# Optimization experiments

Hardware: AMD Instinct MI355X
Metric: run time of the kernel (lower is better)

Reference implementation:

```python
import jax, jax.numpy as jnp
import numpy as np

H = 1024      # hidden_size
NH = 16       # num_attention_heads
HD = H // NH  # head_size
DF = 4096     # ff intermediate
EPS = 1e-5


def layer_norm(x, g, b):
    mu = jnp.mean(x, axis=-1, keepdims=True)
    var = jnp.var(x, axis=-1, keepdims=True)
    return (x - mu) * jax.lax.rsqrt(var + EPS) * g + b


def setup_inputs() -> dict:
    key = jax.random.key(0)
    ks = jax.random.split(key, 4)
    s = 0.02
    return {
        "x": jax.random.normal(ks[0], (2, 2048, H), dtype=jnp.float32),
        "w_qkv": jax.random.normal(ks[1], (H, 3 * H), dtype=jnp.float32) * s,
        "ln1_g": jnp.ones((H,), jnp.float32),
        "ln1_b": jnp.zeros((H,), jnp.float32),
        "w1": jax.random.normal(ks[2], (H, DF), dtype=jnp.float32) * s,
        "b1": jnp.zeros((DF,), jnp.float32),
        "w2": jax.random.normal(ks[3], (DF, H), dtype=jnp.float32) * s,
        "b2": jnp.zeros((H,), jnp.float32),
        "ln2_g": jnp.ones((H,), jnp.float32),
        "ln2_b": jnp.zeros((H,), jnp.float32),
    }


def reference(x, w_qkv, ln1_g, ln1_b, w1, b1, w2, b2, ln2_g, ln2_b):
    b, s, h = x.shape
    # --- MHSelfAttention (naive) ---
    qkv = x @ w_qkv                                   # [b, s, 3h]
    qkv = qkv.reshape(b, s, 3, NH, HD)
    q, k, v = (jnp.moveaxis(qkv, 2, 0)                # [3, b, s, nh, hd]
               .transpose(0, 1, 3, 2, 4))             # [3, b, nh, s, hd]
    # NOTE: faithful quirk — scaled by sqrt(hidden_size), not head_size
    scores = jnp.einsum('bnqd,bnkd->bnqk', q, k) / jnp.sqrt(jnp.float32(h))
    probs = jax.nn.softmax(scores, axis=-1)
    ctx = jnp.einsum('bnqk,bnkd->bnqd', probs, v)     # [b, nh, s, hd]
    attn_out = ctx.transpose(0, 2, 1, 3).reshape(b, s, h)
    # post-norm residual (dropout = identity in eval)
    x = x + layer_norm(attn_out, ln1_g, ln1_b)
    # --- FFN ---
    ff = jax.nn.relu(x @ w1 + b1) @ w2 + b2
    x = x + layer_norm(ff, ln2_g, ln2_b)
    return x
```

## Files before the change

### kernel.cpp

```cpp
#include <hip/hip_runtime.h>


typedef unsigned short u16;
typedef unsigned int u32;
typedef __bf16 bf16x8 __attribute__((ext_vector_type(8)));
typedef float f32x4 __attribute__((ext_vector_type(4)));
typedef float f32x16 __attribute__((ext_vector_type(16)));
typedef u32 u32x4 __attribute__((ext_vector_type(4)));
typedef u16 u16x4 __attribute__((ext_vector_type(4)));

__device__ __forceinline__ u16 f2b(float f) {
  u32 u = __builtin_bit_cast(u32, f);
  u += 0x7fffu + ((u >> 16) & 1u);
  return (u16)(u >> 16);
}
__device__ __forceinline__ float b2f(u16 u) {
  return __builtin_bit_cast(float, (u32)u << 16);
}

__device__ __forceinline__ u32 cvtpk(float lo, float hi) {
  u32 r;
  asm("v_cvt_pk_bf16_f32 %0, %1, %2" : "=v"(r) : "v"(lo), "v"(hi));
  return r;
}

__device__ __forceinline__ void gld_lds16(const u16* g, u16* l) {
  __builtin_amdgcn_global_load_lds(
      (const __attribute__((address_space(1))) u32*)g,
      (__attribute__((address_space(3))) u32*)l, 16, 0, 0);
}

__global__ __launch_bounds__(256) void convert_bf16_kernel(
    const float* __restrict__ in, u16* __restrict__ out) {
  const int idx = blockIdx.x * 256 + threadIdx.x;
  float4 v = ((const float4*)in)[idx];
  u16x4 o = { f2b(v.x), f2b(v.y), f2b(v.z), f2b(v.w) };
  ((u16x4*)out)[idx] = o;
}

__global__ __launch_bounds__(256) void transpose_bf16_kernel(
    const float* __restrict__ in, u16* __restrict__ out, int R, int C) {
  __shared__ float tile[32][33];
  const int cb = blockIdx.x * 32, rb = blockIdx.y * 32;
  const int c = threadIdx.x & 31;
  const int r0 = threadIdx.x >> 5;
#pragma unroll
  for (int rr = 0; rr < 32; rr += 8)
    tile[r0 + rr][c] = in[(size_t)(rb + r0 + rr) * C + cb + c];
  __syncthreads();
#pragma unroll
  for (int rr = 0; rr < 32; rr += 8)
    out[(size_t)(cb + r0 + rr) * R + rb + c] = f2b(tile[c][r0 + rr]);
}

__global__ __launch_bounds__(256) void transpose_v_kernel(
    const u16* __restrict__ qkv, u16* __restrict__ vt) {
  __shared__ u16 t[64][70];
  const int bh = blockIdx.x, st = blockIdx.y;
  const int b = bh >> 4, nh = bh & 15;
  const int s0 = st * 64;
  const int r = threadIdx.x >> 3, c = (threadIdx.x & 7) << 3;
  const u16* src = qkv + (size_t)(b * 2048 + s0) * 3072 + 2048 + nh * 64;
#pragma unroll
  for (int rr = 0; rr < 64; rr += 32)
    *(u32x4*)&t[r + rr][c] = *(const u32x4*)(src + (size_t)(r + rr) * 3072 + c);
  __syncthreads();
  u16* dst = vt + ((size_t)bh * 64) * 2048 + s0;
#pragma unroll
  for (int rr = 0; rr < 64; rr += 32) {
    const int d = r + rr;
    u16 tmp[8];
#pragma unroll
    for (int j = 0; j < 8; ++j) tmp[j] = t[c + j][d];
    *(u32x4*)(dst + (size_t)d * 2048 + c) = *(u32x4*)tmp;
  }
}

__global__ __launch_bounds__(256) void gemm_bt_kernel(
    const u16* __restrict__ A, const u16* __restrict__ Bt,
    const float* __restrict__ bias, float* __restrict__ Cf, u16* __restrict__ Cb,
    int M, int N, int K, int relu,
    u16* __restrict__ Cb1, u16* __restrict__ Cb2, u16* __restrict__ Cb3) {
  const int bid = blockIdx.x;
  const int xcd = bid & 7;
  const int g = bid >> 3;
  const int m0 = (xcd * 4 + (g & 3)) * 128;
  const int n0 = (g >> 2) * 128;
  const int z = blockIdx.y;
  const int kn = K / (int)gridDim.y;
  if (z == 1) Cb = Cb1; else if (z == 2) Cb = Cb2; else if (z == 3) Cb = Cb3;
  const int tid = threadIdx.x;
  const int w = tid >> 6, lane = tid & 63, quad = lane >> 4, l16 = lane & 15;
  const int wm = (w & 1) * 64, wn = (w >> 1) * 64;

  __shared__ u16 As[2][128][32];
  __shared__ u16 Bs[2][128][32];

  f32x4 acc[4][4];
#pragma unroll
  for (int i = 0; i < 4; ++i)
#pragma unroll
    for (int j = 0; j < 4; ++j) acc[i][j] = {0.f, 0.f, 0.f, 0.f};

  const int srow = w * 16 + (lane >> 2);
  const int scol = (lane & 3) << 3;
  const u16* Ag = A + (size_t)(m0 + srow) * K + scol + (size_t)z * kn;
  const u16* Bg = Bt + (size_t)(n0 + srow) * K + scol + (size_t)z * kn;
  const size_t rstep = (size_t)64 * K;

  for (int k0 = 0; k0 < kn; k0 += 64) {
    __syncthreads();
    gld_lds16(Ag + k0,              &As[0][w * 16][0]);
    gld_lds16(Ag + k0 + 32,         &As[1][w * 16][0]);
    gld_lds16(Ag + rstep + k0,      &As[0][64 + w * 16][0]);
    gld_lds16(Ag + rstep + k0 + 32, &As[1][64 + w * 16][0]);
    gld_lds16(Bg + k0,              &Bs[0][w * 16][0]);
    gld_lds16(Bg + k0 + 32,         &Bs[1][w * 16][0]);
    gld_lds16(Bg + rstep + k0,      &Bs[0][64 + w * 16][0]);
    gld_lds16(Bg + rstep + k0 + 32, &Bs[1][64 + w * 16][0]);
    __syncthreads();

#pragma unroll
    for (int s = 0; s < 2; ++s) {
      bf16x8 af[4], bfr[4];
#pragma unroll
      for (int i = 0; i < 4; ++i)
        af[i] = *(const bf16x8*)&As[s][wm + i * 16 + l16][quad * 8];
#pragma unroll
      for (int j = 0; j < 4; ++j)
        bfr[j] = *(const bf16x8*)&Bs[s][wn + j * 16 + l16][quad * 8];
#pragma unroll
      for (int i = 0; i < 4; ++i)
#pragma unroll
        for (int j = 0; j < 4; ++j)
          acc[i][j] = __builtin_amdgcn_mfma_f32_16x16x32_bf16(af[i], bfr[j], acc[i][j], 0, 0, 0);
    }
  }

#pragma unroll
  for (int i = 0; i < 4; ++i) {
    const int row = m0 + wm + i * 16 + quad * 4;
#pragma unroll
    for (int j = 0; j < 4; ++j) {
      const int col = n0 + wn + j * 16 + l16;
      const float bv = bias ? bias[col] : 0.f;
#pragma unroll
      for (int r = 0; r < 4; ++r) {
        float v = acc[i][j][r] + bv;
        if (relu) v = fmaxf(v, 0.f);
        const size_t idx = (size_t)(row + r) * N + col;
        if (Cf) Cf[idx] = v;
        if (Cb) Cb[idx] = f2b(v);
      }
    }
  }
}

__global__ __launch_bounds__(256, 4) void attn_kernel(
    const u16* __restrict__ qkv, const u16* __restrict__ vt,
    float* __restrict__ Op0, float* __restrict__ Op1,
    float* __restrict__ lpart) {
  const int bh = blockIdx.x;
  const int qt = blockIdx.y;
  const int kz = blockIdx.z;
  const int b = bh >> 4, nh = bh & 15;
  const int tid = threadIdx.x;
  const int w = tid >> 6, lane = tid & 63;
  const int l32 = lane & 31, hi = lane >> 5;
  const float c2 = 0.04508422f;

  __shared__ u16 KS[64][64];
  __shared__ u16 VS[64][64];

  const size_t rs = 3072;
  const u16* qbase = qkv + (size_t)b * 2048 * rs + nh * 64;
  const u16* kbase = qbase + 1024;
  const u16* vbase = vt + (size_t)bh * 64 * 2048;
  const int q0 = qt * 128;
  const int k0beg = kz * 1024;

  bf16x8 aq[4];
  {
    const u16* qrow = qbase + (size_t)(q0 + w * 32 + l32) * rs + hi * 8;
#pragma unroll
    for (int ds = 0; ds < 4; ++ds) {
      u32x4 v = *(const u32x4*)(qrow + ds * 16);
      u16 ti[8], to[8];
      *(u32x4*)ti = v;
#pragma unroll
      for (int j = 0; j < 8; ++j) to[j] = f2b(b2f(ti[j]) * c2);
      u32x4 pk = *(u32x4*)to;
      aq[ds] = __builtin_bit_cast(bf16x8, pk);
    }
  }

  f32x16 Oacc[2];
#pragma unroll
  for (int dn = 0; dn < 2; ++dn)
#pragma unroll
    for (int i = 0; i < 16; ++i) Oacc[dn][i] = 0.f;
  float ls[4] = {0.f, 0.f, 0.f, 0.f};

  const int srow = lane >> 3;
  const int scol = ((lane & 7) ^ srow) << 3;

#pragma unroll 1
  for (int t = 0; t < 16; ++t) {
    const int k0 = k0beg + t * 64;
    __syncthreads();
    gld_lds16(kbase + (size_t)(k0 + w * 16 + srow) * rs + scol,       &KS[w * 16][0]);
    gld_lds16(kbase + (size_t)(k0 + w * 16 + 8 + srow) * rs + scol,   &KS[w * 16 + 8][0]);
    gld_lds16(vbase + (size_t)(w * 16 + srow) * 2048 + k0 + scol,     &VS[w * 16][0]);
    gld_lds16(vbase + (size_t)(w * 16 + 8 + srow) * 2048 + k0 + scol, &VS[w * 16 + 8][0]);
    __syncthreads();

    f32x16 S[2];
#pragma unroll
    for (int jt = 0; jt < 2; ++jt)
#pragma unroll
      for (int i = 0; i < 16; ++i) S[jt][i] = 0.f;
#pragma unroll
    for (int jt = 0; jt < 2; ++jt) {
      const int krow = jt * 32 + l32;
#pragma unroll
      for (int ds = 0; ds < 4; ++ds) {
        bf16x8 kv = *(const bf16x8*)&KS[krow][((2 * ds + hi) ^ (krow & 7)) << 3];
        S[jt] = __builtin_amdgcn_mfma_f32_32x32x16_bf16(kv, aq[ds], S[jt], 0, 0, 0);
      }
    }

    bf16x8 pa[4];
#pragma unroll
    for (int jt = 0; jt < 2; ++jt) {
      float p[16];
#pragma unroll
      for (int r = 0; r < 16; ++r) {
        p[r] = exp2f(S[jt][r]);
        ls[r & 3] += p[r];
      }
#pragma unroll
      for (int bq = 0; bq < 2; ++bq) {
        u32 x0 = cvtpk(p[8 * bq + 0], p[8 * bq + 1]);
        u32 y0 = cvtpk(p[8 * bq + 4], p[8 * bq + 5]);
        u32 x1 = cvtpk(p[8 * bq + 2], p[8 * bq + 3]);
        u32 y1 = cvtpk(p[8 * bq + 6], p[8 * bq + 7]);
        asm("v_permlane32_swap_b32 %0, %1" : "+v"(x0), "+v"(y0));
        asm("v_permlane32_swap_b32 %0, %1" : "+v"(x1), "+v"(y1));
        u32x4 dw = {x0, x1, y0, y1};
        pa[2 * jt + bq] = __builtin_bit_cast(bf16x8, dw);
      }
    }

#pragma unroll
    for (int dn = 0; dn < 2; ++dn) {
      const int vrow = dn * 32 + l32;
#pragma unroll
      for (int ks = 0; ks < 4; ++ks) {
        bf16x8 vv = *(const bf16x8*)&VS[vrow][((2 * ks + hi) ^ (vrow & 7)) << 3];
        Oacc[dn] = __builtin_amdgcn_mfma_f32_32x32x16_bf16(pa[ks], vv, Oacc[dn], 0, 0, 0);
      }
    }
  }

  float lsum = (ls[0] + ls[1]) + (ls[2] + ls[3]);
  const float ltot = lsum + __shfl_xor(lsum, 32);

  float* opart = kz ? Op1 : Op0;
  float* obase = opart + (size_t)b * 2048 * 1024 + (size_t)nh * 64;
  float* lbase = lpart + (size_t)kz * 4096 * 16 + (size_t)b * 2048 * 16 + nh;
#pragma unroll
  for (int r = 0; r < 16; ++r) {
    const int qrow = q0 + w * 32 + (r & 3) + 8 * (r >> 2) + 4 * hi;
#pragma unroll
    for (int dn = 0; dn < 2; ++dn)
      obase[(size_t)qrow * 1024 + dn * 32 + l32] = Oacc[dn][r];
  }
  if (lane < 32) lbase[(size_t)(q0 + w * 32 + l32) * 16] = ltot;
}

__global__ __launch_bounds__(256) void ln_attn_kernel(
    const float* __restrict__ O0, const float* __restrict__ O1,
    const float* __restrict__ l0, const float* __restrict__ l1,
    const float* __restrict__ xres, const float* __restrict__ g,
    const float* __restrict__ bb, float* __restrict__ outf,
    u16* __restrict__ outb) {
  const int row = blockIdx.x;
  const int tid = threadIdx.x;
  const int w = tid >> 6, lane = tid & 63;
  const int head = tid >> 4;
  float4 a0 = ((const float4*)(O0 + (size_t)row * 1024))[tid];
  float4 a1 = ((const float4*)(O1 + (size_t)row * 1024))[tid];
  const float inv = 1.f / (l0[row * 16 + head] + l1[row * 16 + head]);
  float4 v;
  v.x = (a0.x + a1.x) * inv;
  v.y = (a0.y + a1.y) * inv;
  v.z = (a0.z + a1.z) * inv;
  v.w = (a0.w + a1.w) * inv;
  float s = v.x + v.y + v.z + v.w;
  float s2 = v.x * v.x + v.y * v.y + v.z * v.z + v.w * v.w;
#pragma unroll
  for (int off = 32; off > 0; off >>= 1) {
    s += __shfl_xor(s, off);
    s2 += __shfl_xor(s2, off);
  }
  __shared__ float red[8];
  if (lane == 0) { red[w] = s; red[4 + w] = s2; }
  __syncthreads();
  s = red[0] + red[1] + red[2] + red[3];
  s2 = red[4] + red[5] + red[6] + red[7];
  const float mu = s * (1.f / 1024.f);
  const float var = s2 * (1.f / 1024.f) - mu * mu;
  const float rstd = rsqrtf(var + 1e-5f);
  float4 xr = ((const float4*)(xres + (size_t)row * 1024))[tid];
  float4 gv = ((const float4*)g)[tid];
  float4 bv = ((const float4*)bb)[tid];
  float4 o;
  o.x = xr.x + (v.x - mu) * rstd * gv.x + bv.x;
  o.y = xr.y + (v.y - mu) * rstd * gv.y + bv.y;
  o.z = xr.z + (v.z - mu) * rstd * gv.z + bv.z;
  o.w = xr.w + (v.w - mu) * rstd * gv.w + bv.w;
  ((float4*)(outf + (size_t)row * 1024))[tid] = o;
  u16x4 ob = { f2b(o.x), f2b(o.y), f2b(o.z), f2b(o.w) };
  *(u16x4*)(outb + (size_t)row * 1024 + (size_t)tid * 4) = ob;
}

__global__ __launch_bounds__(256) void ln_ffn_kernel(
    const u16* __restrict__ p0, const u16* __restrict__ p1,
    const u16* __restrict__ p2, const u16* __restrict__ p3,
    const float* __restrict__ bias, const float* __restrict__ xres,
    const float* __restrict__ g, const float* __restrict__ bb,
    float* __restrict__ outf) {
  const int row = blockIdx.x;
  const int tid = threadIdx.x;
  const int w = tid >> 6, lane = tid & 63;
  u16x4 a0 = ((const u16x4*)(p0 + (size_t)row * 1024))[tid];
  u16x4 a1 = ((const u16x4*)(p1 + (size_t)row * 1024))[tid];
  u16x4 a2 = ((const u16x4*)(p2 + (size_t)row * 1024))[tid];
  u16x4 a3 = ((const u16x4*)(p3 + (size_t)row * 1024))[tid];
  float4 bv4 = ((const float4*)bias)[tid];
  float4 v;
  v.x = (b2f(a0[0]) + b2f(a1[0])) + (b2f(a2[0]) + b2f(a3[0])) + bv4.x;
  v.y = (b2f(a0[1]) + b2f(a1[1])) + (b2f(a2[1]) + b2f(a3[1])) + bv4.y;
  v.z = (b2f(a0[2]) + b2f(a1[2])) + (b2f(a2[2]) + b2f(a3[2])) + bv4.z;
  v.w = (b2f(a0[3]) + b2f(a1[3])) + (b2f(a2[3]) + b2f(a3[3])) + bv4.w;
  float s = v.x + v.y + v.z + v.w;
  float s2 = v.x * v.x + v.y * v.y + v.z * v.z + v.w * v.w;
#pragma unroll
  for (int off = 32; off > 0; off >>= 1) {
    s += __shfl_xor(s, off);
    s2 += __shfl_xor(s2, off);
  }
  __shared__ float red[8];
  if (lane == 0) { red[w] = s; red[4 + w] = s2; }
  __syncthreads();
  s = red[0] + red[1] + red[2] + red[3];
  s2 = red[4] + red[5] + red[6] + red[7];
  const float mu = s * (1.f / 1024.f);
  const float var = s2 * (1.f / 1024.f) - mu * mu;
  const float rstd = rsqrtf(var + 1e-5f);
  float4 xr = ((const float4*)(xres + (size_t)row * 1024))[tid];
  float4 gv = ((const float4*)g)[tid];
  float4 bv = ((const float4*)bb)[tid];
  float4 o;
  o.x = xr.x + (v.x - mu) * rstd * gv.x + bv.x;
  o.y = xr.y + (v.y - mu) * rstd * gv.y + bv.y;
  o.z = xr.z + (v.z - mu) * rstd * gv.z + bv.z;
  o.w = xr.w + (v.w - mu) * rstd * gv.w + bv.w;
  ((float4*)(outf + (size_t)row * 1024))[tid] = o;
}

extern "C" void kernel_launch(void* const* d_in, const int* in_sizes, int n_in,
                              void* d_out, int out_size, void* d_ws, size_t ws_size,
                              hipStream_t stream) {
  const float* x     = (const float*)d_in[0];
  const float* w_qkv = (const float*)d_in[1];
  const float* ln1_g = (const float*)d_in[2];
  const float* ln1_b = (const float*)d_in[3];
  const float* w1    = (const float*)d_in[4];
  const float* b1    = (const float*)d_in[5];
  const float* w2    = (const float*)d_in[6];
  const float* b2    = (const float*)d_in[7];
  const float* ln2_g = (const float*)d_in[8];
  const float* ln2_b = (const float*)d_in[9];
  float* out = (float*)d_out;
  char* ws = (char*)d_ws;

  u16*   xb    = (u16*)(ws + 0);
  u16*   wqkvT = (u16*)(ws + 8388608);
  u16*   qkvb  = (u16*)(ws + 31457280);
  u16*   vT    = (u16*)(ws + 56623104);
  float* Op0   = (float*)(ws + 0);
  float* Op1   = (float*)(ws + 73400320);
  float* lp    = (float*)(ws + 90177536);
  float* x1    = (float*)(ws + 31457280);
  u16*   x1b   = (u16*)(ws + 48234496);
  u16*   w1T   = (u16*)(ws + 14680064);
  u16*   w2T   = (u16*)(ws + 23068672);
  u16*   h1    = (u16*)(ws + 56623104);
  u16*   fp0   = (u16*)(ws + 0);
  u16*   fp1   = (u16*)(ws + 8388608);
  u16*   fp2   = (u16*)(ws + 48234496);
  u16*   fp3   = (u16*)(ws + 90177536);

  convert_bf16_kernel<<<4096, 256, 0, stream>>>(x, xb);
  transpose_bf16_kernel<<<dim3(96, 32), 256, 0, stream>>>(w_qkv, wqkvT, 1024, 3072);

  gemm_bt_kernel<<<dim3(32 * 24, 1), 256, 0, stream>>>(
      xb, wqkvT, nullptr, nullptr, qkvb, 4096, 3072, 1024, 0,
      nullptr, nullptr, nullptr);
  transpose_v_kernel<<<dim3(32, 32), 256, 0, stream>>>(qkvb, vT);
  attn_kernel<<<dim3(32, 16, 2), 256, 0, stream>>>(qkvb, vT, Op0, Op1, lp);

  ln_attn_kernel<<<4096, 256, 0, stream>>>(
      Op0, Op1, lp, lp + 4096 * 16, x, ln1_g, ln1_b, x1, x1b);

  transpose_bf16_kernel<<<dim3(128, 32), 256, 0, stream>>>(w1, w1T, 1024, 4096);
  transpose_bf16_kernel<<<dim3(32, 128), 256, 0, stream>>>(w2, w2T, 4096, 1024);

  gemm_bt_kernel<<<dim3(32 * 32, 1), 256, 0, stream>>>(
      x1b, w1T, b1, nullptr, h1, 4096, 4096, 1024, 1,
      nullptr, nullptr, nullptr);
  gemm_bt_kernel<<<dim3(32 * 8, 4), 256, 0, stream>>>(
      h1, w2T, nullptr, nullptr, fp0, 4096, 1024, 4096, 0,
      fp1, fp2, fp3);

  ln_ffn_kernel<<<4096, 256, 0, stream>>>(
      fp0, fp1, fp2, fp3, b2, x1, ln2_g, ln2_b, out);
}
```

Before: 344.8 us.

## Double-buffer K/V LDS tiles in attention kernel to overlap loads with MFMA

The attention kernel now keeps two K and two V tiles in shared memory. It issues the direct global-to-LDS loads for the next key block before computing on the current one, and moves the Q-load prologue to overlap with the first stage. Each iteration now has one wait-and-barrier instead of two __syncthreads, which is meant to hide global load latency behind the QK and PV MFMAs. LDS use doubles to 32 KB per block, which could reduce occupancy relative to the declared 4 blocks per CU.

```diff
diff --git a/kernel.cpp b/kernel.cpp
--- a/kernel.cpp
+++ b/kernel.cpp
@@ -169,8 +169,8 @@
   const int l32 = lane & 31, hi = lane >> 5;
   const float c2 = 0.04508422f;
 
-  __shared__ u16 KS[64][64];
-  __shared__ u16 VS[64][64];
+  __shared__ u16 KS[2][64][64];
+  __shared__ u16 VS[2][64][64];
 
   const size_t rs = 3072;
   const u16* qbase = qkv + (size_t)b * 2048 * rs + nh * 64;
@@ -179,6 +179,18 @@
   const int q0 = qt * 128;
   const int k0beg = kz * 1024;
 
+  const int srow = lane >> 3;
+  const int scol = ((lane & 7) ^ srow) << 3;
+
+  auto stage = [&](int buf, int k0) {
+    gld_lds16(kbase + (size_t)(k0 + w * 16 + srow) * rs + scol,       &KS[buf][w * 16][0]);
+    gld_lds16(kbase + (size_t)(k0 + w * 16 + 8 + srow) * rs + scol,   &KS[buf][w * 16 + 8][0]);
+    gld_lds16(vbase + (size_t)(w * 16 + srow) * 2048 + k0 + scol,     &VS[buf][w * 16][0]);
+    gld_lds16(vbase + (size_t)(w * 16 + 8 + srow) * 2048 + k0 + scol, &VS[buf][w * 16 + 8][0]);
+  };
+
+  stage(0, k0beg);
+
   bf16x8 aq[4];
   {
     const u16* qrow = qbase + (size_t)(q0 + w * 32 + l32) * rs + hi * 8;
@@ -201,18 +213,14 @@
     for (int i = 0; i < 16; ++i) Oacc[dn][i] = 0.f;
   float ls[4] = {0.f, 0.f, 0.f, 0.f};
 
-  const int srow = lane >> 3;
-  const int scol = ((lane & 7) ^ srow) << 3;
-
+  asm volatile("s_waitcnt vmcnt(0)" ::: "memory");
+  __builtin_amdgcn_s_barrier();
+  __builtin_amdgcn_sched_barrier(0);
+
+  int cur = 0;
 #pragma unroll 1
   for (int t = 0; t < 16; ++t) {
-    const int k0 = k0beg + t * 64;
-    __syncthreads();
-    gld_lds16(kbase + (size_t)(k0 + w * 16 + srow) * rs + scol,       &KS[w * 16][0]);
-    gld_lds16(kbase + (size_t)(k0 + w * 16 + 8 + srow) * rs + scol,   &KS[w * 16 + 8][0]);
-    gld_lds16(vbase + (size_t)(w * 16 + srow) * 2048 + k0 + scol,     &VS[w * 16][0]);
-    gld_lds16(vbase + (size_t)(w * 16 + 8 + srow) * 2048 + k0 + scol, &VS[w * 16 + 8][0]);
-    __syncthreads();
+    if (t < 15) stage(cur ^ 1, k0beg + (t + 1) * 64);
 
     f32x16 S[2];
 #pragma unroll
@@ -224,7 +232,7 @@
       const int krow = jt * 32 + l32;
 #pragma unroll
       for (int ds = 0; ds < 4; ++ds) {
-        bf16x8 kv = *(const bf16x8*)&KS[krow][((2 * ds + hi) ^ (krow & 7)) << 3];
+        bf16x8 kv = *(const bf16x8*)&KS[cur][krow][((2 * ds + hi) ^ (krow & 7)) << 3];
         S[jt] = __builtin_amdgcn_mfma_f32_32x32x16_bf16(kv, aq[ds], S[jt], 0, 0, 0);
       }
     }
@@ -256,10 +264,16 @@
       const int vrow = dn * 32 + l32;
 #pragma unroll
       for (int ks = 0; ks < 4; ++ks) {
-        bf16x8 vv = *(const bf16x8*)&VS[vrow][((2 * ks + hi) ^ (vrow & 7)) << 3];
+        bf16x8 vv = *(const bf16x8*)&VS[cur][vrow][((2 * ks + hi) ^ (vrow & 7)) << 3];
         Oacc[dn] = __builtin_amdgcn_mfma_f32_32x32x16_bf16(pa[ks], vv, Oacc[dn], 0, 0, 0);
       }
     }
+
+    __builtin_amdgcn_sched_barrier(0);
+    asm volatile("s_waitcnt vmcnt(0)" ::: "memory");
+    __builtin_amdgcn_s_barrier();
+    __builtin_amdgcn_sched_barrier(0);
+    cur ^= 1;
   }
 
   float lsum = (ls[0] + ls[1]) + (ls[2] + ls[3]);
```

After: 343.7 us. About the same (-0.3%).

## Split attention key range across wave pairs within block, reduce partials in LDS

Applied to the files above, without the earlier changes.

Each attention block now covers 64 query rows instead of 128. Its four waves form two pairs, and each pair walks half of the block's key range with its own K/V LDS buffers. At the end the second pair's O and row-sum partials go through shared memory to the first pair, which adds them and writes out. The grid doubles so the GPU gets more blocks and shorter serial key loops per block, at the cost of a final LDS reduction, twice the LDS footprint, and more total Q loading per K/V tile.

```diff
diff --git a/kernel.cpp b/kernel.cpp
--- a/kernel.cpp
+++ b/kernel.cpp
@@ -166,22 +166,26 @@
   const int b = bh >> 4, nh = bh & 15;
   const int tid = threadIdx.x;
   const int w = tid >> 6, lane = tid & 63;
+  const int qw = w & 1, kp = w >> 1;
   const int l32 = lane & 31, hi = lane >> 5;
   const float c2 = 0.04508422f;
 
-  __shared__ u16 KS[64][64];
-  __shared__ u16 VS[64][64];
+  __shared__ u16 KS[2][64][64];
+  __shared__ u16 VS[2][64][64];
 
   const size_t rs = 3072;
   const u16* qbase = qkv + (size_t)b * 2048 * rs + nh * 64;
   const u16* kbase = qbase + 1024;
   const u16* vbase = vt + (size_t)bh * 64 * 2048;
-  const int q0 = qt * 128;
-  const int k0beg = kz * 1024;
+  const int q0 = qt * 64;
+  const int k0beg = kz * 1024 + kp * 512;
+
+  const int srow = lane >> 3;
+  const int scol = ((lane & 7) ^ srow) << 3;
 
   bf16x8 aq[4];
   {
-    const u16* qrow = qbase + (size_t)(q0 + w * 32 + l32) * rs + hi * 8;
+    const u16* qrow = qbase + (size_t)(q0 + qw * 32 + l32) * rs + hi * 8;
 #pragma unroll
     for (int ds = 0; ds < 4; ++ds) {
       u32x4 v = *(const u32x4*)(qrow + ds * 16);
@@ -189,6 +193,7 @@
       *(u32x4*)ti = v;
 #pragma unroll
       for (int j = 0; j < 8; ++j) to[j] = f2b(b2f(ti[j]) * c2);
+      *(u32x4*)to = *(u32x4*)to;
       u32x4 pk = *(u32x4*)to;
       aq[ds] = __builtin_bit_cast(bf16x8, pk);
     }
@@ -201,17 +206,16 @@
     for (int i = 0; i < 16; ++i) Oacc[dn][i] = 0.f;
   float ls[4] = {0.f, 0.f, 0.f, 0.f};
 
-  const int srow = lane >> 3;
-  const int scol = ((lane & 7) ^ srow) << 3;
-
 #pragma unroll 1
-  for (int t = 0; t < 16; ++t) {
+  for (int t = 0; t < 8; ++t) {
     const int k0 = k0beg + t * 64;
     __syncthreads();
-    gld_lds16(kbase + (size_t)(k0 + w * 16 + srow) * rs + scol,       &KS[w * 16][0]);
-    gld_lds16(kbase + (size_t)(k0 + w * 16 + 8 + srow) * rs + scol,   &KS[w * 16 + 8][0]);
-    gld_lds16(vbase + (size_t)(w * 16 + srow) * 2048 + k0 + scol,     &VS[w * 16][0]);
-    gld_lds16(vbase + (size_t)(w * 16 + 8 + srow) * 2048 + k0 + scol, &VS[w * 16 + 8][0]);
+#pragma unroll
+    for (int i = 0; i < 4; ++i) {
+      const int rr = qw * 32 + i * 8;
+      gld_lds16(kbase + (size_t)(k0 + rr + srow) * rs + scol,   &KS[kp][rr][0]);
+      gld_lds16(vbase + (size_t)(rr + srow) * 2048 + k0 + scol, &VS[kp][rr][0]);
+    }
     __syncthreads();
 
     f32x16 S[2];
@@ -224,7 +228,7 @@
       const int krow = jt * 32 + l32;
 #pragma unroll
       for (int ds = 0; ds < 4; ++ds) {
-        bf16x8 kv = *(const bf16x8*)&KS[krow][((2 * ds + hi) ^ (krow & 7)) << 3];
+        bf16x8 kv = *(const bf16x8*)&KS[kp][krow][((2 * ds + hi) ^ (krow & 7)) << 3];
         S[jt] = __builtin_amdgcn_mfma_f32_32x32x16_bf16(kv, aq[ds], S[jt], 0, 0, 0);
       }
     }
@@ -256,26 +260,42 @@
       const int vrow = dn * 32 + l32;
 #pragma unroll
       for (int ks = 0; ks < 4; ++ks) {
-        bf16x8 vv = *(const bf16x8*)&VS[vrow][((2 * ks + hi) ^ (vrow & 7)) << 3];
+        bf16x8 vv = *(const bf16x8*)&VS[kp][vrow][((2 * ks + hi) ^ (vrow & 7)) << 3];
         Oacc[dn] = __builtin_amdgcn_mfma_f32_32x32x16_bf16(pa[ks], vv, Oacc[dn], 0, 0, 0);
       }
     }
   }
 
   float lsum = (ls[0] + ls[1]) + (ls[2] + ls[3]);
-  const float ltot = lsum + __shfl_xor(lsum, 32);
-
-  float* opart = kz ? Op1 : Op0;
-  float* obase = opart + (size_t)b * 2048 * 1024 + (size_t)nh * 64;
-  float* lbase = lpart + (size_t)kz * 4096 * 16 + (size_t)b * 2048 * 16 + nh;
-#pragma unroll
-  for (int r = 0; r < 16; ++r) {
-    const int qrow = q0 + w * 32 + (r & 3) + 8 * (r >> 2) + 4 * hi;
-#pragma unroll
-    for (int dn = 0; dn < 2; ++dn)
-      obase[(size_t)qrow * 1024 + dn * 32 + l32] = Oacc[dn][r];
-  }
-  if (lane < 32) lbase[(size_t)(q0 + w * 32 + l32) * 16] = ltot;
+  lsum += __shfl_xor(lsum, 32);
+
+  __syncthreads();
+  float* shO = (float*)&KS[0][0][0];
+  float* shL = (float*)&VS[0][0][0];
+  if (kp == 1) {
+#pragma unroll
+    for (int r = 0; r < 16; ++r) {
+      const int qr = (r & 3) + 8 * (r >> 2) + 4 * hi;
+      shO[(qw * 32 + qr) * 64 + l32]      = Oacc[0][r];
+      shO[(qw * 32 + qr) * 64 + 32 + l32] = Oacc[1][r];
+    }
+    if (lane < 32) shL[qw * 32 + l32] = lsum;
+  }
+  __syncthreads();
+  if (kp == 0) {
+    float* opart = kz ? Op1 : Op0;
+    float* obase = opart + (size_t)b * 2048 * 1024 + (size_t)nh * 64;
+    float* lbase = lpart + (size_t)kz * 4096 * 16 + (size_t)b * 2048 * 16 + nh;
+#pragma unroll
+    for (int r = 0; r < 16; ++r) {
+      const int qr = (r & 3) + 8 * (r >> 2) + 4 * hi;
+      const int qrow = q0 + qw * 32 + qr;
+      obase[(size_t)qrow * 1024 + l32]      = Oacc[0][r] + shO[(qw * 32 + qr) * 64 + l32];
+      obase[(size_t)qrow * 1024 + 32 + l32] = Oacc[1][r] + shO[(qw * 32 + qr) * 64 + 32 + l32];
+    }
+    if (lane < 32)
+      lbase[(size_t)(q0 + qw * 32 + l32) * 16] = lsum + shL[qw * 32 + l32];
+  }
 }
 
 __global__ __launch_bounds__(256) void ln_attn_kernel(
@@ -409,7 +429,7 @@
       xb, wqkvT, nullptr, nullptr, qkvb, 4096, 3072, 1024, 0,
       nullptr, nullptr, nullptr);
   transpose_v_kernel<<<dim3(32, 32), 256, 0, stream>>>(qkvb, vT);
-  attn_kernel<<<dim3(32, 16, 2), 256, 0, stream>>>(qkvb, vT, Op0, Op1, lp);
+  attn_kernel<<<dim3(32, 32, 2), 256, 0, stream>>>(qkvb, vT, Op0, Op1, lp);
 
   ln_attn_kernel<<<4096, 256, 0, stream>>>(
       Op0, Op1, lp, lp + 4096 * 16, x, ln1_g, ln1_b, x1, x1b);
```

Result: no change. 348.2 us (+1.0%).

## Replace 128x128 GEMM with 256x256 tile, 4-stage pipelined LDS, swizzled layout

Applied to the files above, without the earlier changes.

Replaces the 128x128, 256-thread GEMM with a 256x256 tile kernel using 512 threads and 8x4 accumulator fragments per wave. K is streamed in 32-wide slices through a 4-buffer LDS ring with prefetch two slices ahead. The schedule is explicit, using sched barriers, s_setprio around MFMA bursts and manual vmcnt/lgkmcnt waits. LDS columns are XOR-swizzled to cut bank conflicts, and the block order is remapped across XCDs. The loop trip count is hardcoded to 32 slices, so it assumes a K of 1024 per split. The large tile uses 128KB LDS and many registers, which limits occupancy to one block per CU, and the QKV and W2 GEMMs launch fewer blocks than there are CUs.

```diff
diff --git a/kernel.cpp b/kernel.cpp
--- a/kernel.cpp
+++ b/kernel.cpp
@@ -76,81 +76,120 @@
   }
 }
 
-__global__ __launch_bounds__(256) void gemm_bt_kernel(
+#define GTILE(T, BUF, T2, VM)                                                 \
+  {                                                                           \
+    const u16(*Ab)[32] = As[BUF];                                             \
+    const u16(*Bb)[32] = Bs[BUF];                                             \
+    bf16x8 af[4], bf[4];                                                      \
+    _Pragma("unroll") for (int nr = 0; nr < 4; ++nr)                          \
+        bf[nr] = *(const bf16x8*)&Bb[wn * 64 + nr * 16 + l16][cRd];           \
+    _Pragma("unroll") for (int mr = 0; mr < 4; ++mr)                          \
+        af[mr] = *(const bf16x8*)&Ab[wm * 128 + mr * 16 + l16][cRd];          \
+    if ((T2) >= 0) {                                                          \
+      gld_lds16(Ag + (size_t)(T2) * 32,         &As[(T2) & 3][w * 16][0]);    \
+      gld_lds16(Ag + rstep + (size_t)(T2) * 32, &As[(T2) & 3][128 + w * 16][0]);\
+    }                                                                         \
+    __builtin_amdgcn_sched_barrier(0);                                        \
+    __builtin_amdgcn_s_barrier();                                             \
+    asm volatile("s_waitcnt lgkmcnt(0)" ::: "memory");                        \
+    __builtin_amdgcn_sched_barrier(0);                                        \
+    __builtin_amdgcn_s_setprio(1);                                            \
+    _Pragma("unroll") for (int mr = 0; mr < 4; ++mr)                          \
+        _Pragma("unroll") for (int nr = 0; nr < 4; ++nr)                      \
+            acc[mr][nr] = __builtin_amdgcn_mfma_f32_16x16x32_bf16(            \
+                af[mr], bf[nr], acc[mr][nr], 0, 0, 0);                        \
+    __builtin_amdgcn_s_setprio(0);                                            \
+    __builtin_amdgcn_s_barrier();                                             \
+    _Pragma("unroll") for (int mr = 0; mr < 4; ++mr)                          \
+        af[mr] = *(const bf16x8*)&Ab[wm * 128 + 64 + mr * 16 + l16][cRd];     \
+    if ((T2) >= 0) {                                                          \
+      gld_lds16(Bg + (size_t)(T2) * 32,         &Bs[(T2) & 3][w * 16][0]);    \
+      gld_lds16(Bg + rstep + (size_t)(T2) * 32, &Bs[(T2) & 3][128 + w * 16][0]);\
+    }                                                                         \
+    __builtin_amdgcn_sched_barrier(0);                                        \
+    __builtin_amdgcn_s_barrier();                                             \
+    asm volatile("s_waitcnt lgkmcnt(0)" ::: "memory");                        \
+    __builtin_amdgcn_sched_barrier(0);                                        \
+    __builtin_amdgcn_s_setprio(1);                                            \
+    _Pragma("unroll") for (int mr = 0; mr < 4; ++mr)                          \
+        _Pragma("unroll") for (int nr = 0; nr < 4; ++nr)                      \
+            acc[4 + mr][nr] = __builtin_amdgcn_mfma_f32_16x16x32_bf16(        \
+                af[mr], bf[nr], acc[4 + mr][nr], 0, 0, 0);                    \
+    __builtin_amdgcn_s_setprio(0);                                            \
+    if ((VM) == 4) asm volatile("s_waitcnt vmcnt(4)" ::: "memory");           \
+    else if ((VM) == 0) asm volatile("s_waitcnt vmcnt(0)" ::: "memory");      \
+    __builtin_amdgcn_s_barrier();                                             \
+  }
+
+__global__ __launch_bounds__(512) void gemm256_kernel(
     const u16* __restrict__ A, const u16* __restrict__ Bt,
-    const float* __restrict__ bias, float* __restrict__ Cf, u16* __restrict__ Cb,
+    const float* __restrict__ bias, u16* __restrict__ Cb,
     int M, int N, int K, int relu,
     u16* __restrict__ Cb1, u16* __restrict__ Cb2, u16* __restrict__ Cb3) {
-  const int bid = blockIdx.x;
-  const int xcd = bid & 7;
-  const int g = bid >> 3;
-  const int m0 = (xcd * 4 + (g & 3)) * 128;
-  const int n0 = (g >> 2) * 128;
+  const int nN = N >> 8;
+  const int lin = (blockIdx.x & 7) * ((int)gridDim.x >> 3) + (blockIdx.x >> 3);
+  const int m0 = (lin / nN) << 8;
+  const int n0 = (lin % nN) << 8;
   const int z = blockIdx.y;
-  const int kn = K / (int)gridDim.y;
   if (z == 1) Cb = Cb1; else if (z == 2) Cb = Cb2; else if (z == 3) Cb = Cb3;
+
   const int tid = threadIdx.x;
-  const int w = tid >> 6, lane = tid & 63, quad = lane >> 4, l16 = lane & 15;
-  const int wm = (w & 1) * 64, wn = (w >> 1) * 64;
-
-  __shared__ u16 As[2][128][32];
-  __shared__ u16 Bs[2][128][32];
-
-  f32x4 acc[4][4];
-#pragma unroll
-  for (int i = 0; i < 4; ++i)
+  const int w = tid >> 6, lane = tid & 63;
+  const int quad = lane >> 4, l16 = lane & 15;
+  const int wm = w >> 2, wn = w & 3;
+
+  __shared__ u16 As[4][256][32];
+  __shared__ u16 Bs[4][256][32];
+
+  f32x4 acc[8][4];
+#pragma unroll
+  for (int i = 0; i < 8; ++i)
 #pragma unroll
     for (int j = 0; j < 4; ++j) acc[i][j] = {0.f, 0.f, 0.f, 0.f};
 
-  const int srow = w * 16 + (lane >> 2);
-  const int scol = (lane & 3) << 3;
-  const u16* Ag = A + (size_t)(m0 + srow) * K + scol + (size_t)z * kn;
-  const u16* Bg = Bt + (size_t)(n0 + srow) * K + scol + (size_t)z * kn;
-  const size_t rstep = (size_t)64 * K;
-
-  for (int k0 = 0; k0 < kn; k0 += 64) {
-    __syncthreads();
-    gld_lds16(Ag + k0,              &As[0][w * 16][0]);
-    gld_lds16(Ag + k0 + 32,         &As[1][w * 16][0]);
-    gld_lds16(Ag + rstep + k0,      &As[0][64 + w * 16][0]);
-    gld_lds16(Ag + rstep + k0 + 32, &As[1][64 + w * 16][0]);
-    gld_lds16(Bg + k0,              &Bs[0][w * 16][0]);
-    gld_lds16(Bg + k0 + 32,         &Bs[1][w * 16][0]);
-    gld_lds16(Bg + rstep + k0,      &Bs[0][64 + w * 16][0]);
-    gld_lds16(Bg + rstep + k0 + 32, &Bs[1][64 + w * 16][0]);
-    __syncthreads();
-
-#pragma unroll
-    for (int s = 0; s < 2; ++s) {
-      bf16x8 af[4], bfr[4];
-#pragma unroll
-      for (int i = 0; i < 4; ++i)
-        af[i] = *(const bf16x8*)&As[s][wm + i * 16 + l16][quad * 8];
-#pragma unroll
-      for (int j = 0; j < 4; ++j)
-        bfr[j] = *(const bf16x8*)&Bs[s][wn + j * 16 + l16][quad * 8];
-#pragma unroll
-      for (int i = 0; i < 4; ++i)
-#pragma unroll
-        for (int j = 0; j < 4; ++j)
-          acc[i][j] = __builtin_amdgcn_mfma_f32_16x16x32_bf16(af[i], bfr[j], acc[i][j], 0, 0, 0);
-    }
-  }
-
-#pragma unroll
-  for (int i = 0; i < 4; ++i) {
-    const int row = m0 + wm + i * 16 + quad * 4;
-#pragma unroll
-    for (int j = 0; j < 4; ++j) {
-      const int col = n0 + wn + j * 16 + l16;
+  const int srow = lane >> 2;
+  const int scol = (((lane & 3) ^ (srow & 3)) << 3);
+  const u16* Ag = A + (size_t)(m0 + w * 16 + srow) * K + (size_t)z * 1024 + scol;
+  const u16* Bg = Bt + (size_t)(n0 + w * 16 + srow) * K + (size_t)z * 1024 + scol;
+  const size_t rstep = (size_t)128 * K;
+
+  const int cRd = ((quad ^ (l16 & 3)) << 3);
+
+  gld_lds16(Ag,              &As[0][w * 16][0]);
+  gld_lds16(Ag + rstep,      &As[0][128 + w * 16][0]);
+  gld_lds16(Bg,              &Bs[0][w * 16][0]);
+  gld_lds16(Bg + rstep,      &Bs[0][128 + w * 16][0]);
+  gld_lds16(Ag + 32,         &As[1][w * 16][0]);
+  gld_lds16(Ag + rstep + 32, &As[1][128 + w * 16][0]);
+  gld_lds16(Bg + 32,         &Bs[1][w * 16][0]);
+  gld_lds16(Bg + rstep + 32, &Bs[1][128 + w * 16][0]);
+  asm volatile("s_waitcnt vmcnt(4)" ::: "memory");
+  __builtin_amdgcn_s_barrier();
+
+  for (int tt = 0; tt < 7; ++tt) {
+    const int t = tt * 4;
+    GTILE(t + 0, 0, t + 2, 4)
+    GTILE(t + 1, 1, t + 3, 4)
+    GTILE(t + 2, 2, t + 4, 4)
+    GTILE(t + 3, 3, t + 5, 4)
+  }
+  GTILE(28, 0, 30, 4)
+  GTILE(29, 1, 31, 4)
+  GTILE(30, 2, -1, 0)
+  GTILE(31, 3, -1, -1)
+
+#pragma unroll
+  for (int mr = 0; mr < 8; ++mr) {
+    const int row = m0 + wm * 128 + mr * 16 + quad * 4;
+#pragma unroll
+    for (int nr = 0; nr < 4; ++nr) {
+      const int col = n0 + wn * 64 + nr * 16 + l16;
       const float bv = bias ? bias[col] : 0.f;
 #pragma unroll
       for (int r = 0; r < 4; ++r) {
-        float v = acc[i][j][r] + bv;
+        float v = acc[mr][nr][r] + bv;
         if (relu) v = fmaxf(v, 0.f);
-        const size_t idx = (size_t)(row + r) * N + col;
-        if (Cf) Cf[idx] = v;
-        if (Cb) Cb[idx] = f2b(v);
+        Cb[(size_t)(row + r) * N + col] = f2b(v);
       }
     }
   }
@@ -405,8 +444,8 @@
   convert_bf16_kernel<<<4096, 256, 0, stream>>>(x, xb);
   transpose_bf16_kernel<<<dim3(96, 32), 256, 0, stream>>>(w_qkv, wqkvT, 1024, 3072);
 
-  gemm_bt_kernel<<<dim3(32 * 24, 1), 256, 0, stream>>>(
-      xb, wqkvT, nullptr, nullptr, qkvb, 4096, 3072, 1024, 0,
+  gemm256_kernel<<<dim3(192, 1), 512, 0, stream>>>(
+      xb, wqkvT, nullptr, qkvb, 4096, 3072, 1024, 0,
       nullptr, nullptr, nullptr);
   transpose_v_kernel<<<dim3(32, 32), 256, 0, stream>>>(qkvb, vT);
   attn_kernel<<<dim3(32, 16, 2), 256, 0, stream>>>(qkvb, vT, Op0, Op1, lp);
@@ -417,11 +456,11 @@
   transpose_bf16_kernel<<<dim3(128, 32), 256, 0, stream>>>(w1, w1T, 1024, 4096);
   transpose_bf16_kernel<<<dim3(32, 128), 256, 0, stream>>>(w2, w2T, 4096, 1024);
 
-  gemm_bt_kernel<<<dim3(32 * 32, 1), 256, 0, stream>>>(
-      x1b, w1T, b1, nullptr, h1, 4096, 4096, 1024, 1,
+  gemm256_kernel<<<dim3(256, 1), 512, 0, stream>>>(
+      x1b, w1T, b1, h1, 4096, 4096, 1024, 1,
       nullptr, nullptr, nullptr);
-  gemm_bt_kernel<<<dim3(32 * 8, 4), 256, 0, stream>>>(
-      h1, w2T, nullptr, nullptr, fp0, 4096, 1024, 4096, 0,
+  gemm256_kernel<<<dim3(64, 4), 512, 0, stream>>>(
+      h1, w2T, nullptr, fp0, 4096, 1024, 4096, 0,
       fp1, fp2, fp3);
 
   ln_ffn_kernel<<<4096, 256, 0, stream>>>(
```

Result: faster. 325.7 us (-5.6%).
